# Performance work log

Hardware: AMD Instinct MI355X
Metric: run time of the kernel (lower is better)

## Reference

```python
import jax, jax.numpy as jnp
import numpy as np
from jax import lax

QMAX = 127.0
EPS = 1e-8

T, B, I, H, L = 1024, 16, 1024, 1024, 2


def setup_inputs() -> dict:
    key = jax.random.key(0)
    ks = jax.random.split(key, 16)
    d = {
        "x": jax.random.normal(ks[0], (T, B, I), jnp.float32),
        "h0": jnp.zeros((L, B, H), jnp.float32),
        "c0": jnp.zeros((L, B, H), jnp.float32),
    }
    # layer 0 weights
    d["w_ih0"] = jax.random.normal(ks[1], (4 * H, I), jnp.float32) * 0.05
    d["w_hh0"] = jax.random.normal(ks[2], (4 * H, H), jnp.float32) * 0.05
    d["b_ih0"] = jax.random.normal(ks[3], (4 * H,), jnp.float32) * 0.05
    d["b_hh0"] = jax.random.normal(ks[4], (4 * H,), jnp.float32) * 0.05
    # layer 1 weights (layer_input_size == hidden_size)
    d["w_ih1"] = jax.random.normal(ks[5], (4 * H, H), jnp.float32) * 0.05
    d["w_hh1"] = jax.random.normal(ks[6], (4 * H, H), jnp.float32) * 0.05
    d["b_ih1"] = jax.random.normal(ks[7], (4 * H,), jnp.float32) * 0.05
    d["b_hh1"] = jax.random.normal(ks[8], (4 * H,), jnp.float32) * 0.05
    return d


def _quantize_weight(w):
    # per-tensor symmetric int8 quantization (simulates quantized.linear_prepack)
    s = jnp.maximum(jnp.max(jnp.abs(w)), EPS) / QMAX
    wq = jnp.clip(jnp.round(w / s), -QMAX, QMAX)  # integer values held in fp32
    return wq, s


def _dynq_matmul(x, wq, w_scale):
    # dynamic per-tensor activation quantization + int8xint8 matmul (fp32-emulated)
    x_scale = jnp.maximum(jnp.max(jnp.abs(x)), EPS) / QMAX
    xq = jnp.clip(jnp.round(x / x_scale), -QMAX, QMAX)
    return (xq @ wq.T) * (x_scale * w_scale)


def _lstm_layer(x, h0, c0, w_ih, w_hh, b_ih, b_hh):
    wq_ih, s_ih = _quantize_weight(w_ih)
    wq_hh, s_hh = _quantize_weight(w_hh)

    def step(carry, xt):
        h, c = carry
        gates = (_dynq_matmul(xt, wq_ih, s_ih) + b_ih
                 + _dynq_matmul(h, wq_hh, s_hh) + b_hh)  # [B, 4H]
        i, f, g, o = jnp.split(gates, 4, axis=-1)  # PyTorch gate order i,f,g,o
        i, f, o = jax.nn.sigmoid(i), jax.nn.sigmoid(f), jax.nn.sigmoid(o)
        g = jnp.tanh(g)
        c_new = f * c + i * g
        h_new = o * jnp.tanh(c_new)
        return (h_new, c_new), h_new

    (hT, cT), ys = lax.scan(step, (h0, c0), x)
    return ys, hT, cT


def reference(x, h0, c0, w_ih0, w_hh0, b_ih0, b_hh0, w_ih1, w_hh1, b_ih1, b_hh1):
    y, h_l0, c_l0 = _lstm_layer(x, h0[0], c0[0], w_ih0, w_hh0, b_ih0, b_hh0)
    y, h_l1, c_l1 = _lstm_layer(y, h0[1], c0[1], w_ih1, w_hh1, b_ih1, b_hh1)
    h_n = jnp.stack([h_l0, h_l1], axis=0)  # [L, B, H]
    c_n = jnp.stack([c_l0, c_l1], axis=0)
    return y, h_n, c_n
```

## Files before the change

### kernel.cpp

```cpp
#include <hip/hip_runtime.h>


#define T_STEPS 1024

typedef int v4i __attribute__((ext_vector_type(4)));
typedef float v4f __attribute__((ext_vector_type(4)));

#define DEV static __device__ __forceinline__

DEV float qclip(float v) { return fminf(fmaxf(v, -127.0f), 127.0f); }

DEV unsigned pack4i(float a, float b, float c, float d) {
  int ia = (int)a, ib = (int)b, ic = (int)c, id = (int)d;
  return (unsigned)(ia & 0xff) | ((unsigned)(ib & 0xff) << 8) |
         ((unsigned)(ic & 0xff) << 16) | ((unsigned)(id & 0xff) << 24);
}

DEV float qdiv(float v, float s) { return qclip(rintf(v / s)); }
DEV float qmul(float v, float inv) { return qclip(rintf(v * inv)); }

DEV v4i cloadi(const void* p) {
  v4i r;
  asm volatile("global_load_dwordx4 %0, %1, off sc0 sc1" : "=v"(r) : "v"(p) : "memory");
  return r;
}
DEV v4f cloadf(const void* p) {
  v4f r;
  asm volatile("global_load_dwordx4 %0, %1, off sc0 sc1" : "=v"(r) : "v"(p) : "memory");
  return r;
}
DEV void cstore16(void* p, v4f v) {
  asm volatile("global_store_dwordx4 %0, %1, off sc0 sc1" :: "v"(p), "v"(v) : "memory");
}
DEV void cstore4(void* p, unsigned v) {
  asm volatile("global_store_dword %0, %1, off sc0 sc1" :: "v"(p), "v"(v) : "memory");
}
DEV void vdone() {
  asm volatile("s_waitcnt vmcnt(0)" ::: "memory");
  __builtin_amdgcn_sched_barrier(0);
}

DEV unsigned aload(const unsigned* p) {
  return __hip_atomic_load((unsigned*)p, __ATOMIC_RELAXED, __HIP_MEMORY_SCOPE_AGENT);
}
DEV void astore(unsigned* p, unsigned v) {
  __hip_atomic_store(p, v, __ATOMIC_RELAXED, __HIP_MEMORY_SCOPE_AGENT);
}
DEV void amax(unsigned* p, unsigned v) {
  __hip_atomic_fetch_max(p, v, __ATOMIC_RELAXED, __HIP_MEMORY_SCOPE_AGENT);
}

DEV void wait2(const unsigned* fa, unsigned ta, const unsigned* fb, unsigned tb, int tid) {
  if (tid < 64) {
    const unsigned* p = (tid < 32) ? (fa + tid) : (fb ? fb + (tid - 32) : fa + (tid - 32));
    const unsigned tgt = (tid < 32) ? ta : (fb ? tb : 0u);
    unsigned guard = 0;
    for (;;) {
      unsigned v = aload(p);
      if (__ballot(v >= tgt) == ~0ull) break;
      __builtin_amdgcn_s_sleep(1);
      if (++guard > (1u << 18)) break;
    }
  }
  __syncthreads();
}

__global__ void init_kernel(const float* __restrict__ h0in,
                            float* __restrict__ h0f, float* __restrict__ h1f,
                            unsigned* hmax0, unsigned* hmax1) {
  const int layer = blockIdx.x;
  const int tid = threadIdx.x;
  const float* src = h0in + layer * 16384;
  float* dst = (layer ? h1f : h0f) + 16384;
  __shared__ float red[256];
  float m = 0.0f;
  for (int i = tid; i < 16384; i += 256) {
    float v = src[i];
    dst[i] = v;
    m = fmaxf(m, fabsf(v));
  }
  red[tid] = m;
  __syncthreads();
  for (int off = 128; off > 0; off >>= 1) {
    if (tid < off) red[tid] = fmaxf(red[tid], red[tid + off]);
    __syncthreads();
  }
  if (tid == 0) (layer ? hmax1 : hmax0)[0] = __float_as_uint(red[0]);
}

__global__ void wabsmax_kernel(const float* __restrict__ w0, const float* __restrict__ w1,
                               const float* __restrict__ w2, const float* __restrict__ w3,
                               unsigned* wmax) {
  const int tensor = blockIdx.x >> 8;
  const int blk = blockIdx.x & 255;
  const float* w = tensor == 0 ? w0 : tensor == 1 ? w1 : tensor == 2 ? w2 : w3;
  const int tid = threadIdx.x;
  const float4* src = (const float4*)w;
  float m = 0.0f;
#pragma unroll
  for (int i = 0; i < 16; ++i) {
    float4 v = src[blk * 4096 + (i << 8) + tid];
    m = fmaxf(m, fmaxf(fmaxf(fabsf(v.x), fabsf(v.y)), fmaxf(fabsf(v.z), fabsf(v.w))));
  }
  __shared__ float red[256];
  red[tid] = m;
  __syncthreads();
  for (int off = 128; off > 0; off >>= 1) {
    if (tid < off) red[tid] = fmaxf(red[tid], red[tid + off]);
    __syncthreads();
  }
  if (tid == 0)
    __hip_atomic_fetch_max(&wmax[tensor], __float_as_uint(red[0]),
                           __ATOMIC_RELAXED, __HIP_MEMORY_SCOPE_AGENT);
}

__global__ void wquant_kernel(const float* __restrict__ w0, const float* __restrict__ w1,
                              const float* __restrict__ w2, const float* __restrict__ w3,
                              const unsigned* __restrict__ wmax,
                              unsigned char* __restrict__ wq) {
  const int tensor = blockIdx.x >> 12;
  const int blk = blockIdx.x & 4095;
  const float* w = tensor == 0 ? w0 : tensor == 1 ? w1 : tensor == 2 ? w2 : w3;
  const float s = fmaxf(__uint_as_float(wmax[tensor]), 1e-8f) / 127.0f;
  const int f4 = (blk << 8) + threadIdx.x;
  float4 v = ((const float4*)w)[f4];
  unsigned* dst = (unsigned*)(wq + (size_t)tensor * 4194304u);
  dst[f4] = pack4i(qdiv(v.x, s), qdiv(v.y, s), qdiv(v.z, s), qdiv(v.w, s));
}

__global__ void xquant_kernel(const float* __restrict__ x, float* __restrict__ xscale,
                              unsigned char* __restrict__ xq) {
  const int t = blockIdx.x;
  const int tid = threadIdx.x;
  const float4* src = (const float4*)(x + (size_t)t * 16384u);
  float4 vb[16];
  float m = 0.0f;
#pragma unroll
  for (int i = 0; i < 16; ++i) {
    float4 v = src[(i << 8) + tid];
    vb[i] = v;
    m = fmaxf(m, fmaxf(fmaxf(fabsf(v.x), fabsf(v.y)), fmaxf(fabsf(v.z), fabsf(v.w))));
  }
  __shared__ float red[256];
  red[tid] = m;
  __syncthreads();
  for (int off = 128; off > 0; off >>= 1) {
    if (tid < off) red[tid] = fmaxf(red[tid], red[tid + off]);
    __syncthreads();
  }
  __shared__ float ssh;
  if (tid == 0) {
    float s = fmaxf(red[0], 1e-8f) / 127.0f;
    xscale[t] = s;
    ssh = s;
  }
  __syncthreads();
  const float s = ssh;
  unsigned* dst = (unsigned*)(xq + (size_t)t * 16384u);
#pragma unroll
  for (int i = 0; i < 16; ++i) {
    float4 v = vb[i];
    dst[(i << 8) + tid] = pack4i(qdiv(v.x, s), qdiv(v.y, s), qdiv(v.z, s), qdiv(v.w, s));
  }
}

__global__ __launch_bounds__(512, 2) void seq_kernel(
    const unsigned char* __restrict__ xq, const float* __restrict__ xscale,
    const unsigned char* __restrict__ wq_base, const unsigned* __restrict__ wmax,
    const float* __restrict__ bih0, const float* __restrict__ bhh0,
    const float* __restrict__ bih1, const float* __restrict__ bhh1,
    char* __restrict__ ws, const float* __restrict__ c0in, float* __restrict__ dout) {
  const int blk = blockIdx.x;
  const int layer = blk >> 5;
  const int lb = blk & 31;
  const int j0 = lb << 5;
  const int tid = threadIdx.x;
  const int w = tid >> 6;
  const int lane = tid & 63;
  const int g = w & 3;
  const int ch = w >> 2;

  unsigned* flags0 = (unsigned*)(ws + 128);
  unsigned* flags1 = (unsigned*)(ws + 256);
  unsigned* hmax0p = (unsigned*)(ws + 8192);
  unsigned* hmax1p = (unsigned*)(ws + 16384);
  float* h0f = (float*)(ws + 65536);
  float* h1f = (float*)(ws + 196608);
  unsigned char* h0qp = (unsigned char*)(ws + 327680);

  unsigned* myflags = layer ? flags1 : flags0;
  unsigned* myhmax = layer ? hmax1p : hmax0p;
  float* myhf = layer ? h1f : h0f;

  __shared__ __align__(16) unsigned char axq[16][1040];
  __shared__ __align__(16) unsigned char ahq[16][1040];
  __shared__ float gl[4][16][33];
  __shared__ float hstash[16][33];
  __shared__ float redw[8];

  const unsigned char* wqi = wq_base + (size_t)(2 * layer) * 4194304u;
  const unsigned char* wqh = wq_base + (size_t)(2 * layer + 1) * 4194304u;
  const float* bih = layer ? bih1 : bih0;
  const float* bhh = layer ? bhh1 : bhh0;
  const float s_wi = fmaxf(__uint_as_float(wmax[2 * layer + 0]), 1e-8f) / 127.0f;
  const float s_wh = fmaxf(__uint_as_float(wmax[2 * layer + 1]), 1e-8f) / 127.0f;

  const int ncol = (g << 10) + j0 + (ch << 4) + (lane & 15);
  const int ksub = (lane >> 4) << 4;
  const int arow = lane & 15;

  v4i wfi[16], wfh[16];
  {
    const unsigned char* pi = wqi + (size_t)ncol * 1024u + ksub;
    const unsigned char* ph = wqh + (size_t)ncol * 1024u + ksub;
#pragma unroll
    for (int kk = 0; kk < 16; ++kk) {
      wfi[kk] = *(const v4i*)(pi + (kk << 6));
      wfh[kk] = *(const v4i*)(ph + (kk << 6));
    }
  }
  const float bsum = bih[ncol] + bhh[ncol];

  const int cb = tid >> 5, cj = tid & 31;
  float creg = c0in[(layer << 14) + (cb << 10) + j0 + cj];

  if (layer == 0) {
    for (int s = 0; s <= T_STEPS; ++s) {
      const bool full = (s < T_STEPS);
      v4i accx = {0, 0, 0, 0};
      if (full) {
        const v4i* src = (const v4i*)(xq + ((size_t)s << 14));
#pragma unroll
        for (int i = 0; i < 2; ++i) {
          int idx = (i << 9) + tid;
          v4i v = src[idx];
          int e = idx << 4;
          *(v4i*)&axq[e >> 10][e & 1023] = v;
        }
        __syncthreads();
#pragma unroll
        for (int kk = 0; kk < 16; ++kk) {
          v4i a = *(const v4i*)&axq[arow][(kk << 6) + ksub];
          accx = __builtin_amdgcn_mfma_i32_16x16x64_i8(a, wfi[kk], accx, 0, 0, 0);
        }
      }
      const unsigned need1 = (s >= 8) ? (unsigned)(s - 8) : 0u;
      wait2(flags0, (unsigned)s, flags1, need1, tid);

      const float am = __uint_as_float(aload(&hmax0p[s]));
      const float sh = fmaxf(am, 1e-8f) / 127.0f;
      const float inv = 1.0f / sh;

      if (s > 0 && tid < 128) {
        int f = tid << 2, b = f >> 5, c = f & 31;
        unsigned u = pack4i(qmul(hstash[b][c], inv), qmul(hstash[b][c + 1], inv),
                            qmul(hstash[b][c + 2], inv), qmul(hstash[b][c + 3], inv));
        cstore4(h0qp + ((size_t)((s - 1) & 7) << 14) + (b << 10) + j0 + c, u);
      }

      if (full) {
        const char* hsrc = (const char*)(myhf + ((size_t)((s - 1) & 1) << 14));
        v4f hv[8];
#pragma unroll
        for (int i = 0; i < 8; ++i) {
          int idx = (i << 9) + tid;
          hv[i] = cloadf(hsrc + ((size_t)idx << 4));
        }
        vdone();
#pragma unroll
        for (int i = 0; i < 8; ++i) {
          unsigned u = pack4i(qmul(hv[i].x, inv), qmul(hv[i].y, inv),
                              qmul(hv[i].z, inv), qmul(hv[i].w, inv));
          int e = (i << 11) + (tid << 2);
          *(unsigned*)&ahq[e >> 10][e & 1023] = u;
        }
        __syncthreads();
        v4i acch = {0, 0, 0, 0};
#pragma unroll
        for (int kk = 0; kk < 16; ++kk) {
          v4i a = *(const v4i*)&ahq[arow][(kk << 6) + ksub];
          acch = __builtin_amdgcn_mfma_i32_16x16x64_i8(a, wfh[kk], acch, 0, 0, 0);
        }
        const float sx = xscale[s];
        const float fx = sx * s_wi, fh = sh * s_wh;
#pragma unroll
        for (int r = 0; r < 4; ++r) {
          float gate = (float)accx[r] * fx + (float)acch[r] * fh + bsum;
          float act = (g == 2) ? tanhf(gate) : 1.0f / (1.0f + expf(-gate));
          gl[g][((lane >> 4) << 2) + r][(ch << 4) + (lane & 15)] = act;
        }
        __syncthreads();
        float gi = gl[0][cb][cj], gf = gl[1][cb][cj];
        float gg = gl[2][cb][cj], go = gl[3][cb][cj];
        float cnew = gf * creg + gi * gg;
        creg = cnew;
        float h = go * tanhf(cnew);
        hstash[cb][cj] = h;
        float m = fabsf(h);
#pragma unroll
        for (int off = 32; off > 0; off >>= 1) m = fmaxf(m, __shfl_xor(m, off));
        if (lane == 0) redw[w] = m;
        if (s == T_STEPS - 1) dout[16777216u + (cb << 10) + j0 + cj] = h;
        __syncthreads();
        if (tid < 128) {
          int f = tid << 2, b = f >> 5, c = f & 31;
          v4f hw = {hstash[b][c], hstash[b][c + 1], hstash[b][c + 2], hstash[b][c + 3]};
          cstore16(myhf + ((size_t)(s & 1) << 14) + (b << 10) + j0 + c, hw);
        }
        if (tid == 0) {
          float mm = redw[0];
#pragma unroll
          for (int i = 1; i < 8; ++i) mm = fmaxf(mm, redw[i]);
          amax(&hmax0p[s + 1], __float_as_uint(mm));
        }
      }
      vdone();
      __syncthreads();
      if (tid == 0) astore(&flags0[lb], (unsigned)(s + 1));
    }
    dout[16777216u + 32768u + (cb << 10) + j0 + cj] = creg;
  } else {
    for (int u = 0; u < T_STEPS; ++u) {
      wait2(flags0, (unsigned)(u + 2), nullptr, 0u, tid);
      const float sx = fmaxf(__uint_as_float(aload(&hmax0p[u + 1])), 1e-8f) / 127.0f;
      {
        const char* qsrc = (const char*)h0qp + ((size_t)(u & 7) << 14);
        v4i q0 = cloadi(qsrc + ((size_t)tid << 4));
        v4i q1 = cloadi(qsrc + 8192 + ((size_t)tid << 4));
        vdone();
        int e0 = tid << 4;
        *(v4i*)&axq[e0 >> 10][e0 & 1023] = q0;
        int e1 = 8192 + (tid << 4);
        *(v4i*)&axq[e1 >> 10][e1 & 1023] = q1;
      }
      __syncthreads();
      v4i accx = {0, 0, 0, 0};
#pragma unroll
      for (int kk = 0; kk < 16; ++kk) {
        v4i a = *(const v4i*)&axq[arow][(kk << 6) + ksub];
        accx = __builtin_amdgcn_mfma_i32_16x16x64_i8(a, wfi[kk], accx, 0, 0, 0);
      }
      wait2(flags1, (unsigned)u, nullptr, 0u, tid);
      const float sh = fmaxf(__uint_as_float(aload(&hmax1p[u])), 1e-8f) / 127.0f;
      const float inv = 1.0f / sh;
      const char* hsrc = (const char*)(myhf + ((size_t)((u - 1) & 1) << 14));
      v4f hv[8];
#pragma unroll
      for (int i = 0; i < 8; ++i) {
        int idx = (i << 9) + tid;
        hv[i] = cloadf(hsrc + ((size_t)idx << 4));
      }
      vdone();
#pragma unroll
      for (int i = 0; i < 8; ++i) {
        unsigned uq = pack4i(qmul(hv[i].x, inv), qmul(hv[i].y, inv),
                             qmul(hv[i].z, inv), qmul(hv[i].w, inv));
        int e = (i << 11) + (tid << 2);
        *(unsigned*)&ahq[e >> 10][e & 1023] = uq;
      }
      __syncthreads();
      v4i acch = {0, 0, 0, 0};
#pragma unroll
      for (int kk = 0; kk < 16; ++kk) {
        v4i a = *(const v4i*)&ahq[arow][(kk << 6) + ksub];
        acch = __builtin_amdgcn_mfma_i32_16x16x64_i8(a, wfh[kk], acch, 0, 0, 0);
      }
      const float fx = sx * s_wi, fh = sh * s_wh;
#pragma unroll
      for (int r = 0; r < 4; ++r) {
        float gate = (float)accx[r] * fx + (float)acch[r] * fh + bsum;
        float act = (g == 2) ? tanhf(gate) : 1.0f / (1.0f + expf(-gate));
        gl[g][((lane >> 4) << 2) + r][(ch << 4) + (lane & 15)] = act;
      }
      __syncthreads();
      float gi = gl[0][cb][cj], gf = gl[1][cb][cj];
      float gg = gl[2][cb][cj], go = gl[3][cb][cj];
      float cnew = gf * creg + gi * gg;
      creg = cnew;
      float h = go * tanhf(cnew);
      hstash[cb][cj] = h;
      float m = fabsf(h);
#pragma unroll
      for (int off = 32; off > 0; off >>= 1) m = fmaxf(m, __shfl_xor(m, off));
      if (lane == 0) redw[w] = m;
      dout[((size_t)u << 14) + (cb << 10) + j0 + cj] = h;
      if (u == T_STEPS - 1) dout[16777216u + 16384u + (cb << 10) + j0 + cj] = h;
      __syncthreads();
      if (tid < 128) {
        int f = tid << 2, b = f >> 5, c = f & 31;
        v4f hw = {hstash[b][c], hstash[b][c + 1], hstash[b][c + 2], hstash[b][c + 3]};
        cstore16(myhf + ((size_t)(u & 1) << 14) + (b << 10) + j0 + c, hw);
      }
      if (tid == 0) {
        float mm = redw[0];
#pragma unroll
        for (int i = 1; i < 8; ++i) mm = fmaxf(mm, redw[i]);
        amax(&hmax1p[u + 1], __float_as_uint(mm));
      }
      vdone();
      __syncthreads();
      if (tid == 0) astore(&flags1[lb], (unsigned)(u + 1));
    }
    dout[16777216u + 32768u + 16384u + (cb << 10) + j0 + cj] = creg;
  }
}

extern "C" void kernel_launch(void* const* d_in, const int* in_sizes, int n_in,
                              void* d_out, int out_size, void* d_ws, size_t ws_size,
                              hipStream_t stream) {
  (void)in_sizes; (void)n_in; (void)out_size; (void)ws_size;
  const float* x     = (const float*)d_in[0];
  const float* h0in  = (const float*)d_in[1];
  const float* c0in  = (const float*)d_in[2];
  const float* w_ih0 = (const float*)d_in[3];
  const float* w_hh0 = (const float*)d_in[4];
  const float* b_ih0 = (const float*)d_in[5];
  const float* b_hh0 = (const float*)d_in[6];
  const float* w_ih1 = (const float*)d_in[7];
  const float* w_hh1 = (const float*)d_in[8];
  const float* b_ih1 = (const float*)d_in[9];
  const float* b_hh1 = (const float*)d_in[10];

  char* ws = (char*)d_ws;
  unsigned* wmax   = (unsigned*)(ws + 0);
  float* xscale    = (float*)(ws + 1024);
  unsigned* hmax0  = (unsigned*)(ws + 8192);
  unsigned* hmax1  = (unsigned*)(ws + 16384);
  float* h0f       = (float*)(ws + 65536);
  float* h1f       = (float*)(ws + 196608);
  unsigned char* wqb = (unsigned char*)(ws + (1u << 20));
  unsigned char* xq  = (unsigned char*)(ws + (1u << 20) + 4u * 4194304u);

  hipMemsetAsync(ws, 0, 65536, stream);
  hipLaunchKernelGGL(init_kernel, dim3(2), dim3(256), 0, stream,
                     h0in, h0f, h1f, hmax0, hmax1);
  hipLaunchKernelGGL(wabsmax_kernel, dim3(1024), dim3(256), 0, stream,
                     w_ih0, w_hh0, w_ih1, w_hh1, wmax);
  hipLaunchKernelGGL(wquant_kernel, dim3(16384), dim3(256), 0, stream,
                     w_ih0, w_hh0, w_ih1, w_hh1, wmax, wqb);
  hipLaunchKernelGGL(xquant_kernel, dim3(1024), dim3(256), 0, stream,
                     x, xscale, xq);
  hipLaunchKernelGGL(seq_kernel, dim3(64), dim3(512), 0, stream,
                     xq, xscale, wqb, wmax,
                     b_ih0, b_hh0, b_ih1, b_hh1,
                     ws, c0in, (float*)d_out);
}
```

Before: 5.540 ms.

## Replace flag/atomic-max sync with packed step+max publish slots and in-register gate combine

Replaces the separate per-block step flags and atomic-max hmax arrays with double-buffered per-block 8-byte slots holding the step counter and that block's partial absmax, which consumers poll and reduce themselves. The gate-to-lane mapping is rearranged so each wave holds all four gates of a unit, which lets the cell update use shuffles instead of LDS round trips and two syncthreads per step. Layer 0 reads x straight from global memory into registers, and MFMA chains are split into two accumulators for more ILP. The aim is a shorter per-step critical path through the recurrence. In exchange, waiters do more polling work and the double-buffered slots depend on a subtle ordering between producer and consumer steps.

```diff
diff --git a/kernel.cpp b/kernel.cpp
--- a/kernel.cpp
+++ b/kernel.cpp
@@ -5,6 +5,7 @@
 
 typedef int v4i __attribute__((ext_vector_type(4)));
 typedef float v4f __attribute__((ext_vector_type(4)));
+typedef unsigned v2u __attribute__((ext_vector_type(2)));
 
 #define DEV static __device__ __forceinline__
 
@@ -29,63 +30,62 @@
   asm volatile("global_load_dwordx4 %0, %1, off sc0 sc1" : "=v"(r) : "v"(p) : "memory");
   return r;
 }
+DEV unsigned cload4(const void* p) {
+  unsigned r;
+  asm volatile("global_load_dword %0, %1, off sc0 sc1" : "=v"(r) : "v"(p) : "memory");
+  return r;
+}
+DEV v2u cload8w(const void* p) {
+  v2u r;
+  asm volatile("global_load_dwordx2 %0, %1, off sc0 sc1\n\ts_waitcnt vmcnt(0)"
+               : "=v"(r) : "v"(p) : "memory");
+  return r;
+}
 DEV void cstore16(void* p, v4f v) {
   asm volatile("global_store_dwordx4 %0, %1, off sc0 sc1" :: "v"(p), "v"(v) : "memory");
 }
-DEV void cstore4(void* p, unsigned v) {
+DEV void cstore8(void* p, v2u v) {
+  asm volatile("global_store_dwordx2 %0, %1, off sc0 sc1" :: "v"(p), "v"(v) : "memory");
+}
+DEV void cstore4f(void* p, float v) {
   asm volatile("global_store_dword %0, %1, off sc0 sc1" :: "v"(p), "v"(v) : "memory");
+}
+DEV void cstoreb(void* p, unsigned v) {
+  asm volatile("global_store_byte %0, %1, off sc0 sc1" :: "v"(p), "v"(v) : "memory");
 }
 DEV void vdone() {
   asm volatile("s_waitcnt vmcnt(0)" ::: "memory");
   __builtin_amdgcn_sched_barrier(0);
 }
 
-DEV unsigned aload(const unsigned* p) {
-  return __hip_atomic_load((unsigned*)p, __ATOMIC_RELAXED, __HIP_MEMORY_SCOPE_AGENT);
-}
-DEV void astore(unsigned* p, unsigned v) {
-  __hip_atomic_store(p, v, __ATOMIC_RELAXED, __HIP_MEMORY_SCOPE_AGENT);
-}
-DEV void amax(unsigned* p, unsigned v) {
-  __hip_atomic_fetch_max(p, v, __ATOMIC_RELAXED, __HIP_MEMORY_SCOPE_AGENT);
-}
-
-DEV void wait2(const unsigned* fa, unsigned ta, const unsigned* fb, unsigned tb, int tid) {
-  if (tid < 64) {
-    const unsigned* p = (tid < 32) ? (fa + tid) : (fb ? fb + (tid - 32) : fa + (tid - 32));
-    const unsigned tgt = (tid < 32) ? ta : (fb ? tb : 0u);
-    unsigned guard = 0;
-    for (;;) {
-      unsigned v = aload(p);
-      if (__ballot(v >= tgt) == ~0ull) break;
-      __builtin_amdgcn_s_sleep(1);
-      if (++guard > (1u << 18)) break;
-    }
-  }
-  __syncthreads();
-}
-
-__global__ void init_kernel(const float* __restrict__ h0in,
-                            float* __restrict__ h0f, float* __restrict__ h1f,
-                            unsigned* hmax0, unsigned* hmax1) {
+#define MFMA_I8 __builtin_amdgcn_mfma_i32_16x16x64_i8
+
+__global__ void init_kernel(const float* __restrict__ h0in, char* __restrict__ ws) {
   const int layer = blockIdx.x;
   const int tid = threadIdx.x;
   const float* src = h0in + layer * 16384;
-  float* dst = (layer ? h1f : h0f) + 16384;
+  float* ring = (float*)(ws + (layer ? 196608 : 65536)) + 16384;
+  v2u* pubs = (v2u*)(ws + (layer ? 640 : 128)) + 32;
+  for (int i = tid; i < 4096; i += 256) {
+    v4f v = ((const v4f*)src)[i];
+    cstore16((char*)ring + ((size_t)i << 4), v);
+  }
   __shared__ float red[256];
+  const int lb = tid >> 3, su = tid & 7;
   float m = 0.0f;
-  for (int i = tid; i < 16384; i += 256) {
-    float v = src[i];
-    dst[i] = v;
-    m = fmaxf(m, fabsf(v));
-  }
+  for (int b = su * 2; b < su * 2 + 2; ++b)
+    for (int q = 0; q < 32; ++q) m = fmaxf(m, fabsf(src[b * 1024 + lb * 32 + q]));
   red[tid] = m;
   __syncthreads();
-  for (int off = 128; off > 0; off >>= 1) {
-    if (tid < off) red[tid] = fmaxf(red[tid], red[tid + off]);
-    __syncthreads();
-  }
-  if (tid == 0) (layer ? hmax1 : hmax0)[0] = __float_as_uint(red[0]);
+  if (su == 0) {
+    float mm = red[tid];
+#pragma unroll
+    for (int i = 1; i < 8; ++i) mm = fmaxf(mm, red[tid + i]);
+    v2u p;
+    p.x = 0u;
+    p.y = __float_as_uint(mm);
+    cstore8((char*)&pubs[lb], p);
+  }
 }
 
 __global__ void wabsmax_kernel(const float* __restrict__ w0, const float* __restrict__ w1,
@@ -177,35 +177,27 @@
   const int tid = threadIdx.x;
   const int w = tid >> 6;
   const int lane = tid & 63;
-  const int g = w & 3;
-  const int ch = w >> 2;
-
-  unsigned* flags0 = (unsigned*)(ws + 128);
-  unsigned* flags1 = (unsigned*)(ws + 256);
-  unsigned* hmax0p = (unsigned*)(ws + 8192);
-  unsigned* hmax1p = (unsigned*)(ws + 16384);
+  const int gate = (lane >> 2) & 3;
+  const int unit = j0 + (w << 2) + (lane & 3);
+  const int b0 = (lane >> 4) << 2;
+
+  v2u* pubs0 = (v2u*)(ws + 128);
+  v2u* pubs1 = (v2u*)(ws + 640);
+  unsigned* hmax0f = (unsigned*)(ws + 4096);
   float* h0f = (float*)(ws + 65536);
   float* h1f = (float*)(ws + 196608);
   unsigned char* h0qp = (unsigned char*)(ws + 327680);
 
-  unsigned* myflags = layer ? flags1 : flags0;
-  unsigned* myhmax = layer ? hmax1p : hmax0p;
-  float* myhf = layer ? h1f : h0f;
-
+  __shared__ __align__(16) unsigned char ahq[16][1040];
   __shared__ __align__(16) unsigned char axq[16][1040];
-  __shared__ __align__(16) unsigned char ahq[16][1040];
-  __shared__ float gl[4][16][33];
-  __shared__ float hstash[16][33];
   __shared__ float redw[8];
 
   const unsigned char* wqi = wq_base + (size_t)(2 * layer) * 4194304u;
   const unsigned char* wqh = wq_base + (size_t)(2 * layer + 1) * 4194304u;
-  const float* bih = layer ? bih1 : bih0;
-  const float* bhh = layer ? bhh1 : bhh0;
   const float s_wi = fmaxf(__uint_as_float(wmax[2 * layer + 0]), 1e-8f) / 127.0f;
   const float s_wh = fmaxf(__uint_as_float(wmax[2 * layer + 1]), 1e-8f) / 127.0f;
 
-  const int ncol = (g << 10) + j0 + (ch << 4) + (lane & 15);
+  const int ncol = (gate << 10) + unit;
   const int ksub = (lane >> 4) << 4;
   const int arow = lane & 15;
 
@@ -219,189 +211,263 @@
       wfh[kk] = *(const v4i*)(ph + (kk << 6));
     }
   }
-  const float bsum = bih[ncol] + bhh[ncol];
-
-  const int cb = tid >> 5, cj = tid & 31;
-  float creg = c0in[(layer << 14) + (cb << 10) + j0 + cj];
+  const float bsum = (layer ? bih1 : bih0)[ncol] + (layer ? bhh1 : bhh0)[ncol];
+
+  float cr[4], hpv[4] = {0.f, 0.f, 0.f, 0.f};
+#pragma unroll
+  for (int r = 0; r < 4; ++r) cr[r] = c0in[(layer << 14) + ((b0 + r) << 10) + unit];
+
+  const int gbase = lane & ~12;
 
   if (layer == 0) {
     for (int s = 0; s <= T_STEPS; ++s) {
       const bool full = (s < T_STEPS);
-      v4i accx = {0, 0, 0, 0};
+      v4i ax0 = {0, 0, 0, 0}, ax1 = {0, 0, 0, 0};
+      float sxs = 0.f;
       if (full) {
-        const v4i* src = (const v4i*)(xq + ((size_t)s << 14));
-#pragma unroll
-        for (int i = 0; i < 2; ++i) {
-          int idx = (i << 9) + tid;
-          v4i v = src[idx];
-          int e = idx << 4;
-          *(v4i*)&axq[e >> 10][e & 1023] = v;
-        }
-        __syncthreads();
-#pragma unroll
-        for (int kk = 0; kk < 16; ++kk) {
-          v4i a = *(const v4i*)&axq[arow][(kk << 6) + ksub];
-          accx = __builtin_amdgcn_mfma_i32_16x16x64_i8(a, wfi[kk], accx, 0, 0, 0);
-        }
-      }
-      const unsigned need1 = (s >= 8) ? (unsigned)(s - 8) : 0u;
-      wait2(flags0, (unsigned)s, flags1, need1, tid);
-
-      const float am = __uint_as_float(aload(&hmax0p[s]));
-      const float sh = fmaxf(am, 1e-8f) / 127.0f;
+        sxs = xscale[s];
+        const unsigned char* xb = xq + ((size_t)s << 14) + (arow << 10) + ksub;
+        v4i xa[8];
+#pragma unroll
+        for (int kk = 0; kk < 8; ++kk) xa[kk] = *(const v4i*)(xb + (kk << 6));
+#pragma unroll
+        for (int kk = 0; kk < 8; kk += 2) {
+          ax0 = MFMA_I8(xa[kk], wfi[kk], ax0, 0, 0, 0);
+          ax1 = MFMA_I8(xa[kk + 1], wfi[kk + 1], ax1, 0, 0, 0);
+        }
+#pragma unroll
+        for (int kk = 0; kk < 8; ++kk) xa[kk] = *(const v4i*)(xb + ((kk + 8) << 6));
+#pragma unroll
+        for (int kk = 0; kk < 8; kk += 2) {
+          ax0 = MFMA_I8(xa[kk], wfi[kk + 8], ax0, 0, 0, 0);
+          ax1 = MFMA_I8(xa[kk + 1], wfi[kk + 9], ax1, 0, 0, 0);
+        }
+      }
+      const v2u* pp;
+      unsigned tgt;
+      if (lane < 32) {
+        pp = pubs0 + (((s + 1) & 1) << 5) + lane;
+        tgt = (unsigned)s;
+      } else {
+        int slot = (s >= 9) ? ((s - 9) & 1) : 0;
+        pp = pubs1 + (slot << 5) + (lane - 32);
+        tgt = (s >= 9) ? (unsigned)(s - 8) : 0u;
+      }
+      v2u pv;
+      unsigned guard = 0;
+      for (;;) {
+        pv = cload8w(pp);
+        if (__ballot(pv.x >= tgt) == ~0ull) break;
+        __builtin_amdgcn_s_sleep(1);
+        if (++guard > (1u << 20)) break;
+      }
+      float pm = __uint_as_float(pv.y);
+#pragma unroll
+      for (int m = 1; m < 32; m <<= 1) pm = fmaxf(pm, __shfl_xor(pm, m));
+      const float gmax = __shfl(pm, 0);
+      const float sh = fmaxf(gmax, 1e-8f) / 127.0f;
       const float inv = 1.0f / sh;
 
-      if (s > 0 && tid < 128) {
-        int f = tid << 2, b = f >> 5, c = f & 31;
-        unsigned u = pack4i(qmul(hstash[b][c], inv), qmul(hstash[b][c + 1], inv),
-                            qmul(hstash[b][c + 2], inv), qmul(hstash[b][c + 3], inv));
-        cstore4(h0qp + ((size_t)((s - 1) & 7) << 14) + (b << 10) + j0 + c, u);
-      }
-
+      v4f hv[8];
       if (full) {
-        const char* hsrc = (const char*)(myhf + ((size_t)((s - 1) & 1) << 14));
-        v4f hv[8];
-#pragma unroll
-        for (int i = 0; i < 8; ++i) {
-          int idx = (i << 9) + tid;
-          hv[i] = cloadf(hsrc + ((size_t)idx << 4));
-        }
-        vdone();
+        const char* hsrc = (const char*)(h0f + ((size_t)((s + 1) & 1) << 14));
+#pragma unroll
+        for (int i = 0; i < 8; ++i) hv[i] = cloadf(hsrc + ((size_t)(((i << 9) + tid)) << 4));
+      }
+      if (s > 0) {
+        if (gate == 0) {
+          unsigned char* qb = h0qp + ((size_t)((s - 1) & 7) << 14) + unit;
+#pragma unroll
+          for (int r = 0; r < 4; ++r) {
+            int q = (int)qmul(hpv[r], inv);
+            cstoreb(qb + ((b0 + r) << 10), (unsigned)(q & 0xff));
+          }
+        }
+        if (lb == 0 && tid == 0) cstore4f((char*)&hmax0f[s - 1], gmax);
+      }
+      vdone();
+      if (full) {
 #pragma unroll
         for (int i = 0; i < 8; ++i) {
           unsigned u = pack4i(qmul(hv[i].x, inv), qmul(hv[i].y, inv),
                               qmul(hv[i].z, inv), qmul(hv[i].w, inv));
-          int e = (i << 11) + (tid << 2);
+          int e = ((i << 9) + tid) << 2;
           *(unsigned*)&ahq[e >> 10][e & 1023] = u;
         }
         __syncthreads();
-        v4i acch = {0, 0, 0, 0};
-#pragma unroll
-        for (int kk = 0; kk < 16; ++kk) {
+        v4i ah0 = {0, 0, 0, 0}, ah1 = {0, 0, 0, 0};
+#pragma unroll
+        for (int kk = 0; kk < 16; kk += 2) {
           v4i a = *(const v4i*)&ahq[arow][(kk << 6) + ksub];
-          acch = __builtin_amdgcn_mfma_i32_16x16x64_i8(a, wfh[kk], acch, 0, 0, 0);
-        }
-        const float sx = xscale[s];
-        const float fx = sx * s_wi, fh = sh * s_wh;
+          v4i b = *(const v4i*)&ahq[arow][((kk + 1) << 6) + ksub];
+          ah0 = MFMA_I8(a, wfh[kk], ah0, 0, 0, 0);
+          ah1 = MFMA_I8(b, wfh[kk + 1], ah1, 0, 0, 0);
+        }
+        const float fx = sxs * s_wi, fh = sh * s_wh;
+        float am = 0.f;
 #pragma unroll
         for (int r = 0; r < 4; ++r) {
-          float gate = (float)accx[r] * fx + (float)acch[r] * fh + bsum;
-          float act = (g == 2) ? tanhf(gate) : 1.0f / (1.0f + expf(-gate));
-          gl[g][((lane >> 4) << 2) + r][(ch << 4) + (lane & 15)] = act;
-        }
-        __syncthreads();
-        float gi = gl[0][cb][cj], gf = gl[1][cb][cj];
-        float gg = gl[2][cb][cj], go = gl[3][cb][cj];
-        float cnew = gf * creg + gi * gg;
-        creg = cnew;
-        float h = go * tanhf(cnew);
-        hstash[cb][cj] = h;
-        float m = fabsf(h);
-#pragma unroll
-        for (int off = 32; off > 0; off >>= 1) m = fmaxf(m, __shfl_xor(m, off));
-        if (lane == 0) redw[w] = m;
-        if (s == T_STEPS - 1) dout[16777216u + (cb << 10) + j0 + cj] = h;
-        __syncthreads();
-        if (tid < 128) {
-          int f = tid << 2, b = f >> 5, c = f & 31;
-          v4f hw = {hstash[b][c], hstash[b][c + 1], hstash[b][c + 2], hstash[b][c + 3]};
-          cstore16(myhf + ((size_t)(s & 1) << 14) + (b << 10) + j0 + c, hw);
-        }
-        if (tid == 0) {
-          float mm = redw[0];
-#pragma unroll
-          for (int i = 1; i < 8; ++i) mm = fmaxf(mm, redw[i]);
-          amax(&hmax0p[s + 1], __float_as_uint(mm));
-        }
+          float gv = (float)(ax0[r] + ax1[r]) * fx + (float)(ah0[r] + ah1[r]) * fh + bsum;
+          float xxv = (gate == 2) ? 2.f * gv : gv;
+          float sg = 1.f / (1.f + expf(-xxv));
+          float act = (gate == 2) ? 2.f * sg - 1.f : sg;
+          float gi = __shfl(act, gbase);
+          float gf = __shfl(act, gbase | 4);
+          float gg = __shfl(act, gbase | 8);
+          float go = __shfl(act, gbase | 12);
+          float cn = gf * cr[r] + gi * gg;
+          cr[r] = cn;
+          float th = 2.f / (1.f + expf(-2.f * cn)) - 1.f;
+          float h = go * th;
+          hpv[r] = h;
+          am = fmaxf(am, fabsf(h));
+        }
+        if (gate == 0) {
+          char* hb = (char*)(h0f + ((size_t)(s & 1) << 14)) + (unit << 2);
+#pragma unroll
+          for (int r = 0; r < 4; ++r) cstore4f(hb + ((size_t)(b0 + r) << 12), hpv[r]);
+          if (s == T_STEPS - 1) {
+#pragma unroll
+            for (int r = 0; r < 4; ++r) dout[16777216u + ((b0 + r) << 10) + unit] = hpv[r];
+          }
+        }
+#pragma unroll
+        for (int m = 1; m < 64; m <<= 1) am = fmaxf(am, __shfl_xor(am, m));
+        if (lane == 0) redw[w] = am;
       }
       vdone();
       __syncthreads();
-      if (tid == 0) astore(&flags0[lb], (unsigned)(s + 1));
+      if (tid == 0) {
+        float bm = redw[0];
+#pragma unroll
+        for (int i = 1; i < 8; ++i) bm = fmaxf(bm, redw[i]);
+        v2u pub;
+        pub.x = (unsigned)(s + 1);
+        pub.y = __float_as_uint(bm);
+        cstore8((char*)(pubs0 + ((s & 1) << 5) + lb), pub);
+      }
     }
-    dout[16777216u + 32768u + (cb << 10) + j0 + cj] = creg;
+    if (gate == 0) {
+#pragma unroll
+      for (int r = 0; r < 4; ++r)
+        dout[16777216u + 32768u + ((b0 + r) << 10) + unit] = cr[r];
+    }
   } else {
     for (int u = 0; u < T_STEPS; ++u) {
-      wait2(flags0, (unsigned)(u + 2), nullptr, 0u, tid);
-      const float sx = fmaxf(__uint_as_float(aload(&hmax0p[u + 1])), 1e-8f) / 127.0f;
+      const v2u* pp;
+      unsigned tgt;
+      if (lane < 32) {
+        pp = pubs0 + (((u + 1) & 1) << 5) + lane;
+        tgt = (unsigned)(u + 2);
+      } else {
+        pp = pubs1 + (((u + 1) & 1) << 5) + (lane - 32);
+        tgt = (unsigned)u;
+      }
+      v2u pv;
+      unsigned guard = 0;
+      for (;;) {
+        pv = cload8w(pp);
+        if (__ballot(pv.x >= tgt) == ~0ull) break;
+        __builtin_amdgcn_s_sleep(1);
+        if (++guard > (1u << 20)) break;
+      }
+      float pm = __uint_as_float(pv.y);
+#pragma unroll
+      for (int m = 1; m < 32; m <<= 1) pm = fmaxf(pm, __shfl_xor(pm, m));
+      const float gmax1 = __shfl(pm, 32);
+      const float sh = fmaxf(gmax1, 1e-8f) / 127.0f;
+      const float inv = 1.0f / sh;
+
+      const char* qsrc = (const char*)h0qp + ((size_t)(u & 7) << 14);
+      v4i q0 = cloadi(qsrc + ((size_t)tid << 4));
+      v4i q1 = cloadi(qsrc + 8192 + ((size_t)tid << 4));
+      const char* hsrc = (const char*)(h1f + ((size_t)((u + 1) & 1) << 14));
+      v4f hv[8];
+#pragma unroll
+      for (int i = 0; i < 8; ++i) hv[i] = cloadf(hsrc + ((size_t)(((i << 9) + tid)) << 4));
+      unsigned sxb = cload4((const char*)&hmax0f[u]);
+      vdone();
+      const float sx = fmaxf(__uint_as_float(sxb), 1e-8f) / 127.0f;
       {
-        const char* qsrc = (const char*)h0qp + ((size_t)(u & 7) << 14);
-        v4i q0 = cloadi(qsrc + ((size_t)tid << 4));
-        v4i q1 = cloadi(qsrc + 8192 + ((size_t)tid << 4));
-        vdone();
         int e0 = tid << 4;
         *(v4i*)&axq[e0 >> 10][e0 & 1023] = q0;
         int e1 = 8192 + (tid << 4);
         *(v4i*)&axq[e1 >> 10][e1 & 1023] = q1;
       }
-      __syncthreads();
-      v4i accx = {0, 0, 0, 0};
-#pragma unroll
-      for (int kk = 0; kk < 16; ++kk) {
-        v4i a = *(const v4i*)&axq[arow][(kk << 6) + ksub];
-        accx = __builtin_amdgcn_mfma_i32_16x16x64_i8(a, wfi[kk], accx, 0, 0, 0);
-      }
-      wait2(flags1, (unsigned)u, nullptr, 0u, tid);
-      const float sh = fmaxf(__uint_as_float(aload(&hmax1p[u])), 1e-8f) / 127.0f;
-      const float inv = 1.0f / sh;
-      const char* hsrc = (const char*)(myhf + ((size_t)((u - 1) & 1) << 14));
-      v4f hv[8];
-#pragma unroll
-      for (int i = 0; i < 8; ++i) {
-        int idx = (i << 9) + tid;
-        hv[i] = cloadf(hsrc + ((size_t)idx << 4));
-      }
-      vdone();
 #pragma unroll
       for (int i = 0; i < 8; ++i) {
         unsigned uq = pack4i(qmul(hv[i].x, inv), qmul(hv[i].y, inv),
                              qmul(hv[i].z, inv), qmul(hv[i].w, inv));
-        int e = (i << 11) + (tid << 2);
+        int e = ((i << 9) + tid) << 2;
         *(unsigned*)&ahq[e >> 10][e & 1023] = uq;
       }
       __syncthreads();
-      v4i acch = {0, 0, 0, 0};
-#pragma unroll
-      for (int kk = 0; kk < 16; ++kk) {
-        v4i a = *(const v4i*)&ahq[arow][(kk << 6) + ksub];
-        acch = __builtin_amdgcn_mfma_i32_16x16x64_i8(a, wfh[kk], acch, 0, 0, 0);
+      v4i ax0 = {0, 0, 0, 0}, ax1 = {0, 0, 0, 0};
+      v4i ah0 = {0, 0, 0, 0}, ah1 = {0, 0, 0, 0};
+#pragma unroll
+      for (int kk = 0; kk < 16; kk += 2) {
+        v4i a0 = *(const v4i*)&axq[arow][(kk << 6) + ksub];
+        v4i a1 = *(const v4i*)&axq[arow][((kk + 1) << 6) + ksub];
+        v4i b0v = *(const v4i*)&ahq[arow][(kk << 6) + ksub];
+        v4i b1v = *(const v4i*)&ahq[arow][((kk + 1) << 6) + ksub];
+        ax0 = MFMA_I8(a0, wfi[kk], ax0, 0, 0, 0);
+        ax1 = MFMA_I8(a1, wfi[kk + 1], ax1, 0, 0, 0);
+        ah0 = MFMA_I8(b0v, wfh[kk], ah0, 0, 0, 0);
+        ah1 = MFMA_I8(b1v, wfh[kk + 1], ah1, 0, 0, 0);
       }
       const float fx = sx * s_wi, fh = sh * s_wh;
+      float am = 0.f;
 #pragma unroll
       for (int r = 0; r < 4; ++r) {
-        float gate = (float)accx[r] * fx + (float)acch[r] * fh + bsum;
-        float act = (g == 2) ? tanhf(gate) : 1.0f / (1.0f + expf(-gate));
-        gl[g][((lane >> 4) << 2) + r][(ch << 4) + (lane & 15)] = act;
-      }
-      __syncthreads();
-      float gi = gl[0][cb][cj], gf = gl[1][cb][cj];
-      float gg = gl[2][cb][cj], go = gl[3][cb][cj];
-      float cnew = gf * creg + gi * gg;
-      creg = cnew;
-      float h = go * tanhf(cnew);
-      hstash[cb][cj] = h;
-      float m = fabsf(h);
-#pragma unroll
-      for (int off = 32; off > 0; off >>= 1) m = fmaxf(m, __shfl_xor(m, off));
-      if (lane == 0) redw[w] = m;
-      dout[((size_t)u << 14) + (cb << 10) + j0 + cj] = h;
-      if (u == T_STEPS - 1) dout[16777216u + 16384u + (cb << 10) + j0 + cj] = h;
-      __syncthreads();
-      if (tid < 128) {
-        int f = tid << 2, b = f >> 5, c = f & 31;
-        v4f hw = {hstash[b][c], hstash[b][c + 1], hstash[b][c + 2], hstash[b][c + 3]};
-        cstore16(myhf + ((size_t)(u & 1) << 14) + (b << 10) + j0 + c, hw);
-      }
-      if (tid == 0) {
-        float mm = redw[0];
-#pragma unroll
-        for (int i = 1; i < 8; ++i) mm = fmaxf(mm, redw[i]);
-        amax(&hmax1p[u + 1], __float_as_uint(mm));
-      }
+        float gv = (float)(ax0[r] + ax1[r]) * fx + (float)(ah0[r] + ah1[r]) * fh + bsum;
+        float xxv = (gate == 2) ? 2.f * gv : gv;
+        float sg = 1.f / (1.f + expf(-xxv));
+        float act = (gate == 2) ? 2.f * sg - 1.f : sg;
+        float gi = __shfl(act, gbase);
+        float gf = __shfl(act, gbase | 4);
+        float gg = __shfl(act, gbase | 8);
+        float go = __shfl(act, gbase | 12);
+        float cn = gf * cr[r] + gi * gg;
+        cr[r] = cn;
+        float th = 2.f / (1.f + expf(-2.f * cn)) - 1.f;
+        float h = go * th;
+        hpv[r] = h;
+        am = fmaxf(am, fabsf(h));
+      }
+      if (gate == 0) {
+        char* hb = (char*)(h1f + ((size_t)(u & 1) << 14)) + (unit << 2);
+        float* yb = dout + ((size_t)u << 14) + unit;
+#pragma unroll
+        for (int r = 0; r < 4; ++r) {
+          cstore4f(hb + ((size_t)(b0 + r) << 12), hpv[r]);
+          yb[(size_t)(b0 + r) << 10] = hpv[r];
+        }
+        if (u == T_STEPS - 1) {
+#pragma unroll
+          for (int r = 0; r < 4; ++r)
+            dout[16777216u + 16384u + ((b0 + r) << 10) + unit] = hpv[r];
+        }
+      }
+#pragma unroll
+      for (int m = 1; m < 64; m <<= 1) am = fmaxf(am, __shfl_xor(am, m));
+      if (lane == 0) redw[w] = am;
       vdone();
       __syncthreads();
-      if (tid == 0) astore(&flags1[lb], (unsigned)(u + 1));
+      if (tid == 0) {
+        float bm = redw[0];
+#pragma unroll
+        for (int i = 1; i < 8; ++i) bm = fmaxf(bm, redw[i]);
+        v2u pub;
+        pub.x = (unsigned)(u + 1);
+        pub.y = __float_as_uint(bm);
+        cstore8((char*)(pubs1 + ((u & 1) << 5) + lb), pub);
+      }
     }
-    dout[16777216u + 32768u + 16384u + (cb << 10) + j0 + cj] = creg;
+    if (gate == 0) {
+#pragma unroll
+      for (int r = 0; r < 4; ++r)
+        dout[16777216u + 32768u + 16384u + ((b0 + r) << 10) + unit] = cr[r];
+    }
   }
 }
 
@@ -423,17 +489,12 @@
 
   char* ws = (char*)d_ws;
   unsigned* wmax   = (unsigned*)(ws + 0);
-  float* xscale    = (float*)(ws + 1024);
-  unsigned* hmax0  = (unsigned*)(ws + 8192);
-  unsigned* hmax1  = (unsigned*)(ws + 16384);
-  float* h0f       = (float*)(ws + 65536);
-  float* h1f       = (float*)(ws + 196608);
+  float* xscale    = (float*)(ws + 8192);
   unsigned char* wqb = (unsigned char*)(ws + (1u << 20));
   unsigned char* xq  = (unsigned char*)(ws + (1u << 20) + 4u * 4194304u);
 
   hipMemsetAsync(ws, 0, 65536, stream);
-  hipLaunchKernelGGL(init_kernel, dim3(2), dim3(256), 0, stream,
-                     h0in, h0f, h1f, hmax0, hmax1);
+  hipLaunchKernelGGL(init_kernel, dim3(2), dim3(256), 0, stream, h0in, ws);
   hipLaunchKernelGGL(wabsmax_kernel, dim3(1024), dim3(256), 0, stream,
                      w_ih0, w_hh0, w_ih1, w_hh1, wmax);
   hipLaunchKernelGGL(wquant_kernel, dim3(16384), dim3(256), 0, stream,
```

Result: slower. 8.461 ms (+52.7%).
